# Optimization experiments

Hardware: AMD Instinct MI355X
Metric: run time of the kernel (lower is better)

## Reference

```python
import jax, jax.numpy as jnp
import numpy as np

HID = 1024      # hidden_size (embedding dim, GRU input)
RNN = 1024      # rnn_hidden_size
VOCAB = 50000   # max_node
STEPS = 1024    # num_steps
SOS = 0


def setup_inputs() -> dict:
    key = jax.random.key(0)
    ks = jax.random.split(key, 8)
    s = 0.02
    return {
        "inputs": jax.random.randint(ks[0], (STEPS,), 0, VOCAB),
        "z": jax.random.normal(ks[1], (RNN,), jnp.float32),
        "emb_W": jax.random.uniform(ks[2], (VOCAB, HID), jnp.float32, -0.001, 0.001),
        "out_b": jnp.full((VOCAB,), 0.01, jnp.float32),
        "h2e_W": jax.random.normal(ks[3], (HID, RNN), jnp.float32) * s,
        "h2e_b": jnp.full((HID,), 0.01, jnp.float32),
        "W_ih": jax.random.normal(ks[4], (3 * RNN, HID), jnp.float32) * s,
        "W_hh": jax.random.normal(ks[5], (3 * RNN, RNN), jnp.float32) * s,
        "b_ih": jnp.zeros((3 * RNN,), jnp.float32),
        "b_hh": jnp.zeros((3 * RNN,), jnp.float32),
    }


def reference(inputs, z, emb_W, out_b, h2e_W, h2e_b, W_ih, W_hh, b_ih, b_hh):
    R = RNN

    def gru_cell(h, x):
        gi = W_ih @ x + b_ih          # (3R,)
        gh = W_hh @ h + b_hh          # (3R,)
        r = jax.nn.sigmoid(gi[:R] + gh[:R])
        zg = jax.nn.sigmoid(gi[R:2 * R] + gh[R:2 * R])
        n = jnp.tanh(gi[2 * R:] + r * gh[2 * R:])
        return (1.0 - zg) * n + zg * h

    # teacher forcing: step i consumes token_{i-1} (SOS for i=1), target is inputs[i]
    step_tokens = jnp.concatenate([jnp.array([SOS], dtype=inputs.dtype), inputs[1:-1]])
    targets = inputs[1:]

    def step(h, tok_tgt):
        tok, tgt = tok_tgt
        x = emb_W[tok]                              # embedding lookup (HID,)
        h_new = gru_cell(h, x)                      # (RNN,)
        e = h2e_W @ h_new + h2e_b                   # (HID,)
        logp = jax.nn.log_softmax(emb_W @ e + out_b)  # tied weights, (VOCAB,)
        return h_new, (-logp[tgt], jnp.argmax(logp))

    _, (losses, preds) = jax.lax.scan(step, z, (step_tokens, targets))
    loss = jnp.sum(losses)
    outputs = jnp.zeros((1, inputs.shape[0]), dtype=jnp.int32).at[0, 1:].set(preds.astype(jnp.int32))
    return loss, outputs
```

## Files before the change

### kernel.cpp

```cpp
#include <hip/hip_runtime.h>
#include <math.h>

#define NV      50000
#define T_STEPS 1023
#define KDIM    1024
#define NCH     391
typedef unsigned long long ull;


__global__ __launch_bounds__(256) void k_gather(const int* __restrict__ inputs,
                                                const float* __restrict__ emb,
                                                float* __restrict__ X) {
  const int t = blockIdx.x;
  const int tid = threadIdx.x;
  float4 v = make_float4(0.f, 0.f, 0.f, 0.f);
  if (t < T_STEPS) {
    const int tok = (t == 0) ? 0 : inputs[t];
    v = *(const float4*)&emb[(size_t)tok * KDIM + tid * 4];
  }
  *(float4*)&X[(size_t)t * KDIM + tid * 4] = v;
}

__global__ __launch_bounds__(256) void k_gemm_ffd(const float* __restrict__ A,
                                                  const float* __restrict__ B,
                                                  const float* __restrict__ bias,
                                                  double* __restrict__ C,
                                                  int N, int K) {
  __shared__ float As[32][68];
  __shared__ float Bs[32][68];
  const int tid = threadIdx.x;
  const int bx = blockIdx.x, by = blockIdx.y;
  const int lr = tid >> 2;
  const int lk = (tid & 3) * 8;
  const float* Ap = A + (size_t)(by * 64 + lr) * K + lk;
  const float* Bp = B + (size_t)(bx * 64 + lr) * K + lk;
  const int r0 = (tid >> 4) * 4;
  const int c0 = (tid & 15) * 4;
  double acc[4][4] = {};
  for (int kc = 0; kc < K; kc += 32) {
    const float4 a0 = *(const float4*)(Ap + kc);
    const float4 a1 = *(const float4*)(Ap + kc + 4);
    const float4 b0 = *(const float4*)(Bp + kc);
    const float4 b1 = *(const float4*)(Bp + kc + 4);
    __syncthreads();
    As[lk+0][lr]=a0.x; As[lk+1][lr]=a0.y; As[lk+2][lr]=a0.z; As[lk+3][lr]=a0.w;
    As[lk+4][lr]=a1.x; As[lk+5][lr]=a1.y; As[lk+6][lr]=a1.z; As[lk+7][lr]=a1.w;
    Bs[lk+0][lr]=b0.x; Bs[lk+1][lr]=b0.y; Bs[lk+2][lr]=b0.z; Bs[lk+3][lr]=b0.w;
    Bs[lk+4][lr]=b1.x; Bs[lk+5][lr]=b1.y; Bs[lk+6][lr]=b1.z; Bs[lk+7][lr]=b1.w;
    __syncthreads();
#pragma unroll
    for (int kk = 0; kk < 32; ++kk) {
      const float4 av = *(const float4*)&As[kk][r0];
      const float4 bv = *(const float4*)&Bs[kk][c0];
      const double aa[4] = {av.x, av.y, av.z, av.w};
      const double bb[4] = {bv.x, bv.y, bv.z, bv.w};
#pragma unroll
      for (int i = 0; i < 4; ++i)
#pragma unroll
        for (int j = 0; j < 4; ++j)
          acc[i][j] = fma(aa[i], bb[j], acc[i][j]);
    }
  }
  const int row = by * 64 + r0;
  const int col = bx * 64 + c0;
#pragma unroll
  for (int i = 0; i < 4; ++i)
#pragma unroll
    for (int j = 0; j < 4; ++j)
      C[(size_t)(row + i) * N + col + j] = acc[i][j] + (double)bias[col + j];
}

__global__ __launch_bounds__(256) void k_gemm_dfd(const double* __restrict__ A,
                                                  const float* __restrict__ B,
                                                  const float* __restrict__ bias,
                                                  double* __restrict__ C,
                                                  int N, int K) {
  __shared__ double As[32][68];
  __shared__ float  Bs[32][68];
  const int tid = threadIdx.x;
  const int bx = blockIdx.x, by = blockIdx.y;
  const int lr = tid >> 2;
  const int lk = (tid & 3) * 8;
  const double* Ap = A + (size_t)(by * 64 + lr) * K + lk;
  const float*  Bp = B + (size_t)(bx * 64 + lr) * K + lk;
  const int r0 = (tid >> 4) * 4;
  const int c0 = (tid & 15) * 4;
  double acc[4][4] = {};
  for (int kc = 0; kc < K; kc += 32) {
    double ar[8];
#pragma unroll
    for (int q = 0; q < 8; ++q) ar[q] = Ap[kc + q];
    const float4 b0 = *(const float4*)(Bp + kc);
    const float4 b1 = *(const float4*)(Bp + kc + 4);
    __syncthreads();
#pragma unroll
    for (int q = 0; q < 8; ++q) As[lk + q][lr] = ar[q];
    Bs[lk+0][lr]=b0.x; Bs[lk+1][lr]=b0.y; Bs[lk+2][lr]=b0.z; Bs[lk+3][lr]=b0.w;
    Bs[lk+4][lr]=b1.x; Bs[lk+5][lr]=b1.y; Bs[lk+6][lr]=b1.z; Bs[lk+7][lr]=b1.w;
    __syncthreads();
#pragma unroll
    for (int kk = 0; kk < 32; ++kk) {
      const double aa[4] = {As[kk][r0+0], As[kk][r0+1], As[kk][r0+2], As[kk][r0+3]};
      const float4 bv = *(const float4*)&Bs[kk][c0];
      const double bb[4] = {bv.x, bv.y, bv.z, bv.w};
#pragma unroll
      for (int i = 0; i < 4; ++i)
#pragma unroll
        for (int j = 0; j < 4; ++j)
          acc[i][j] = fma(aa[i], bb[j], acc[i][j]);
    }
  }
  const int row = by * 64 + r0;
  const int col = bx * 64 + c0;
#pragma unroll
  for (int i = 0; i < 4; ++i)
#pragma unroll
    for (int j = 0; j < 4; ++j)
      C[(size_t)(row + i) * N + col + j] = acc[i][j] + (double)bias[col + j];
}

__global__ __launch_bounds__(512, 2) void k_recur(const float* __restrict__ z,
                                                  const float* __restrict__ Whh,
                                                  const float* __restrict__ bhh,
                                                  const double* __restrict__ GI,
                                                  double* __restrict__ H,
                                                  ull* SA, ull* SB) {
  __shared__ double hs[1024];
  const int tid = threadIdx.x;
  const int w = tid >> 6, l = tid & 63;
  const int ibase = blockIdx.x * 16 + w * 2;
  float wreg[6][16];
#pragma unroll
  for (int il = 0; il < 2; ++il)
#pragma unroll
    for (int g = 0; g < 3; ++g) {
      const float* wp = Whh + (size_t)(g * 1024 + ibase + il) * 1024 + l;
#pragma unroll
      for (int m = 0; m < 16; ++m) wreg[il * 3 + g][m] = wp[m * 64];
    }
  double bh[6];
#pragma unroll
  for (int il = 0; il < 2; ++il)
#pragma unroll
    for (int g = 0; g < 3; ++g) bh[il * 3 + g] = (double)bhh[g * 1024 + ibase + il];

  hs[tid]       = (double)z[tid];
  hs[tid + 512] = (double)z[tid + 512];
  double gi[6];
#pragma unroll
  for (int il = 0; il < 2; ++il)
#pragma unroll
    for (int g = 0; g < 3; ++g) gi[il * 3 + g] = GI[g * 1024 + ibase + il];
  __syncthreads();

  for (int t = 0; t < T_STEPS; ++t) {
    const bool more = (t + 1 < T_STEPS);
    const int p = t & 3;
    double s[6] = {0.0, 0.0, 0.0, 0.0, 0.0, 0.0};
#pragma unroll
    for (int m = 0; m < 16; ++m) {
      const double hv = hs[l + 64 * m];
#pragma unroll
      for (int rr = 0; rr < 6; ++rr) s[rr] = fma((double)wreg[rr][m], hv, s[rr]);
    }
#pragma unroll
    for (int rr = 0; rr < 6; ++rr) {
      double v = s[rr];
#pragma unroll
      for (int mk = 32; mk >= 1; mk >>= 1) v += __shfl_xor(v, mk, 64);
      s[rr] = v;
    }
    double hn = 0.0;
    if (l < 2) {
      const int il = l;
      const double r  = 1.0 / (1.0 + exp(-(gi[il * 3 + 0] + s[il * 3 + 0] + bh[il * 3 + 0])));
      const double zg = 1.0 / (1.0 + exp(-(gi[il * 3 + 1] + s[il * 3 + 1] + bh[il * 3 + 1])));
      const double n  = tanh(gi[il * 3 + 2] + r * (s[il * 3 + 2] + bh[il * 3 + 2]));
      hn = (1.0 - zg) * n + zg * hs[ibase + l];
    }
    double gin[6] = {0.0, 0.0, 0.0, 0.0, 0.0, 0.0};
    if (more) {
      const double* gp = GI + (size_t)(t + 1) * 3072;
#pragma unroll
      for (int il = 0; il < 2; ++il)
#pragma unroll
        for (int g = 0; g < 3; ++g) gin[il * 3 + g] = gp[g * 1024 + ibase + il];
    }
    __syncthreads();
    if (l < 2) {
      const int gidx = ibase + l;
      H[(size_t)t * 1024 + gidx] = hn;
      if (more) {
        const ull hb  = (ull)__double_as_longlong(hn);
        const ull tag = ((ull)(t + 1)) << 32;
        __hip_atomic_store(SA + p * 1024 + gidx, tag | (hb >> 32),
                           __ATOMIC_RELAXED, __HIP_MEMORY_SCOPE_AGENT);
        __hip_atomic_store(SB + p * 1024 + gidx, tag | (hb & 0xFFFFFFFFull),
                           __ATOMIC_RELAXED, __HIP_MEMORY_SCOPE_AGENT);
      }
    }
    if (more) {
      const ull want = (ull)(t + 1);
      ull a0, b0, a1, b1;
      while (true) {
        a0 = __hip_atomic_load(SA + p * 1024 + tid,
                               __ATOMIC_RELAXED, __HIP_MEMORY_SCOPE_AGENT);
        b0 = __hip_atomic_load(SB + p * 1024 + tid,
                               __ATOMIC_RELAXED, __HIP_MEMORY_SCOPE_AGENT);
        if ((a0 >> 32) >= want && (b0 >> 32) >= want) break;
        __builtin_amdgcn_s_sleep(1);
      }
      while (true) {
        a1 = __hip_atomic_load(SA + p * 1024 + tid + 512,
                               __ATOMIC_RELAXED, __HIP_MEMORY_SCOPE_AGENT);
        b1 = __hip_atomic_load(SB + p * 1024 + tid + 512,
                               __ATOMIC_RELAXED, __HIP_MEMORY_SCOPE_AGENT);
        if ((a1 >> 32) >= want && (b1 >> 32) >= want) break;
        __builtin_amdgcn_s_sleep(1);
      }
      hs[tid]       = __longlong_as_double((long long)
                        (((a0 & 0xFFFFFFFFull) << 32) | (b0 & 0xFFFFFFFFull)));
      hs[tid + 512] = __longlong_as_double((long long)
                        (((a1 & 0xFFFFFFFFull) << 32) | (b1 & 0xFFFFFFFFull)));
      __syncthreads();
#pragma unroll
      for (int q = 0; q < 6; ++q) gi[q] = gin[q];
    }
  }
}

__global__ __launch_bounds__(256) void k_logits(const double* __restrict__ E,
                                                const float* __restrict__ emb,
                                                const float* __restrict__ out_b,
                                                const int* __restrict__ inputs,
                                                float* __restrict__ candL,
                                                int* __restrict__ candI,
                                                float* __restrict__ Psum,
                                                float* __restrict__ Ttgt) {
  __shared__ double As[128][35];
  __shared__ float  Bs[32][132];
  const int tid = threadIdx.x;
  const int bx = blockIdx.x, by = blockIdx.y;
  const int arow = tid >> 1;
  const int akk  = (tid & 1) * 16;
  const double* Ap = E + (size_t)(by * 128 + arow) * KDIM + akk;
  const int bcol = tid >> 1;
  const int bk   = (tid & 1) * 16;
  const int brow = bx * 128 + bcol;
  const float* Bp = emb + (size_t)brow * KDIM + bk;
  const bool bvalid = (brow < NV);
  const int r0 = (tid >> 4) * 8;
  const int c0 = (tid & 15) * 8;
  double acc[8][8] = {};
  for (int kc = 0; kc < KDIM; kc += 32) {
    double ar[16];
#pragma unroll
    for (int q = 0; q < 16; ++q) ar[q] = Ap[kc + q];
    float4 br[4];
#pragma unroll
    for (int q = 0; q < 4; ++q)
      br[q] = bvalid ? *(const float4*)(Bp + kc + q * 4)
                     : make_float4(0.f, 0.f, 0.f, 0.f);
    __syncthreads();
#pragma unroll
    for (int q = 0; q < 16; ++q) As[arow][akk + q] = ar[q];
#pragma unroll
    for (int q = 0; q < 4; ++q) {
      Bs[bk + q * 4 + 0][bcol] = br[q].x;
      Bs[bk + q * 4 + 1][bcol] = br[q].y;
      Bs[bk + q * 4 + 2][bcol] = br[q].z;
      Bs[bk + q * 4 + 3][bcol] = br[q].w;
    }
    __syncthreads();
#pragma unroll 4
    for (int kk = 0; kk < 32; ++kk) {
      double aa[8];
#pragma unroll
      for (int i = 0; i < 8; ++i) aa[i] = As[r0 + i][kk];
      const float4 bv0 = *(const float4*)&Bs[kk][c0];
      const float4 bv1 = *(const float4*)&Bs[kk][c0 + 4];
      const double bb[8] = {bv0.x, bv0.y, bv0.z, bv0.w,
                            bv1.x, bv1.y, bv1.z, bv1.w};
#pragma unroll
      for (int i = 0; i < 8; ++i)
#pragma unroll
        for (int j = 0; j < 8; ++j)
          acc[i][j] = fma(aa[i], bb[j], acc[i][j]);
    }
  }
  const int colb = bx * 128 + c0;
#pragma unroll
  for (int i = 0; i < 8; ++i) {
    const int s = by * 128 + r0 + i;
    const bool valid = (s < T_STEPS);
    const int tgt = valid ? inputs[s + 1] : -1;
    float L1 = -3e38f, L2 = -3e38f;
    int   i1 = 0x7FFFFFFF, i2 = 0x7FFFFFFF;
    float se = 0.f, tv = -INFINITY;
#pragma unroll
    for (int j = 0; j < 8; ++j) {
      const int v = colb + j;
      if (v < NV) {
        const double lgd = acc[i][j] + (double)out_b[v];
        const float L = (float)lgd;
        se += expf((float)(lgd - 0.01));
        if (v == tgt) tv = (float)lgd;
        if (L > L1 || (L == L1 && v < i1)) { L2 = L1; i2 = i1; L1 = L; i1 = v; }
        else if (L > L2 || (L == L2 && v < i2)) { L2 = L; i2 = v; }
      }
    }
#pragma unroll
    for (int mk = 1; mk <= 8; mk <<= 1) {
      const float oL1 = __shfl_xor(L1, mk, 64); const int oi1 = __shfl_xor(i1, mk, 64);
      const float oL2 = __shfl_xor(L2, mk, 64); const int oi2 = __shfl_xor(i2, mk, 64);
      if (oL1 > L1 || (oL1 == L1 && oi1 < i1)) { L2 = L1; i2 = i1; L1 = oL1; i1 = oi1; }
      else if (oL1 > L2 || (oL1 == L2 && oi1 < i2)) { L2 = oL1; i2 = oi1; }
      if (oL2 > L1 || (oL2 == L1 && oi2 < i1)) { L2 = L1; i2 = i1; L1 = oL2; i1 = oi2; }
      else if (oL2 > L2 || (oL2 == L2 && oi2 < i2)) { L2 = oL2; i2 = oi2; }
      se += __shfl_xor(se, mk, 64);
      tv = fmaxf(tv, __shfl_xor(tv, mk, 64));
    }
    if (((tid & 15) == 0) && valid) {
      const size_t p = (size_t)s * (2 * NCH) + 2 * bx;
      candL[p] = L1;     candI[p] = i1;
      candL[p + 1] = L2; candI[p + 1] = i2;
      atomicAdd(&Psum[s], se);
      if (tv > -1e30f) Ttgt[s] = tv;
    }
  }
}

__global__ __launch_bounds__(256) void k_preds(const float* __restrict__ candL,
                                               const int* __restrict__ candI,
                                               float* __restrict__ out) {
  __shared__ float sL[256];
  __shared__ int   sI[256];
  const int s = blockIdx.x;
  const int tid = threadIdx.x;
  const int n = 2 * NCH;
  const size_t base = (size_t)s * n;
  float m = -3e38f;
  for (int c = tid; c < n; c += 256) m = fmaxf(m, candL[base + c]);
  sL[tid] = m; __syncthreads();
  for (int st = 128; st > 0; st >>= 1) {
    if (tid < st) sL[tid] = fmaxf(sL[tid], sL[tid + st]);
    __syncthreads();
  }
  const float Lmax = sL[0];
  __syncthreads();
  float bq = -3e38f; int bi = 0x7FFFFFFF;
  for (int c = tid; c < n; c += 256) {
    const float L = candL[base + c];
    const int   v = candI[base + c];
    const float d = L - Lmax;
    const float q = d - 10.8125f;
    if (q > bq || (q == bq && v < bi)) { bq = q; bi = v; }
  }
  sL[tid] = bq; sI[tid] = bi; __syncthreads();
  for (int st = 128; st > 0; st >>= 1) {
    if (tid < st) {
      if (sL[tid + st] > sL[tid] ||
          (sL[tid + st] == sL[tid] && sI[tid + st] < sI[tid])) {
        sL[tid] = sL[tid + st]; sI[tid] = sI[tid + st];
      }
    }
    __syncthreads();
  }
  if (tid == 0) out[2 + s] = (float)sI[0];
}

__global__ __launch_bounds__(1024) void k_finish(const float* __restrict__ Psum,
                                                 const float* __restrict__ Ttgt,
                                                 float* __restrict__ out) {
  __shared__ double red[1024];
  const int s = threadIdx.x;
  double ls = 0.0;
  if (s < T_STEPS) ls = 0.01 + log((double)Psum[s]) - (double)Ttgt[s];
  red[s] = ls;
  __syncthreads();
  for (int st = 512; st > 0; st >>= 1) {
    if (s < st) red[s] += red[s + st];
    __syncthreads();
  }
  if (s == 0) out[0] = (float)red[0];
  if (s == 1) out[1] = 0.f;
}

extern "C" void kernel_launch(void* const* d_in, const int* in_sizes, int n_in,
                              void* d_out, int out_size, void* d_ws, size_t ws_size,
                              hipStream_t stream) {
  const int*   inputs = (const int*)  d_in[0];
  const float* z      = (const float*)d_in[1];
  const float* emb    = (const float*)d_in[2];
  const float* out_b  = (const float*)d_in[3];
  const float* h2eW   = (const float*)d_in[4];
  const float* h2eb   = (const float*)d_in[5];
  const float* Wih    = (const float*)d_in[6];
  const float* Whh    = (const float*)d_in[7];
  const float* bih    = (const float*)d_in[8];
  const float* bhh    = (const float*)d_in[9];

  char* ws8 = (char*)d_ws;
  ull*    SA   = (ull*)ws8;
  ull*    SB   = (ull*)(ws8 + 32768);
  float*  Psum = (float*)(ws8 + 66560);
  float*  Ttgt = (float*)(ws8 + 70656);
  float*  X    = (float*)(ws8 + 81920);
  char*   GIb  = ws8 + 81920 + (4u << 20);
  double* GI   = (double*)GIb;
  double* E    = GI;
  float*  candL = (float*)(GIb + (8u << 20));
  int*    candI = (int*)  (GIb + (8u << 20) + 3211264);
  double* H    = (double*)(ws8 + 81920 + (28u << 20));
  float*  out  = (float*)d_out;

  hipMemsetAsync(ws8, 0, 81920, stream);

  k_gather<<<1024, 256, 0, stream>>>(inputs, emb, X);
  k_gemm_ffd<<<dim3(48, 16), 256, 0, stream>>>(X, Wih, bih, GI, 3072, KDIM);
  k_recur<<<64, 512, 0, stream>>>(z, Whh, bhh, GI, H, SA, SB);
  k_gemm_dfd<<<dim3(16, 16), 256, 0, stream>>>(H, h2eW, h2eb, E, KDIM, KDIM);
  k_logits<<<dim3(NCH, 8), 256, 0, stream>>>(E, emb, out_b, inputs,
                                             candL, candI, Psum, Ttgt);
  k_preds<<<T_STEPS, 256, 0, stream>>>(candL, candI, out);
  k_finish<<<1, 1024, 0, stream>>>(Psum, Ttgt, out);
}
```

Before: 9.921 ms.

## Compute logits GEMM in fp32 with fp64 rescoring of near-max candidates

The vocabulary logits GEMM switches from double-precision accumulation to fp32. Only candidates within a small tolerance of the per-row max are recomputed with a double-precision dot product, which preserves argmax tie-breaking. The h2e GEMM additionally writes an fp32 copy of E for this purpose. The recurrence also shrinks its slot ring from 4 to 2 and adds per-block 'done' counters so the buffers can be reused safely. This risks precision differences in the softmax sum and adds serialization and atomics to the logits epilogue.

```diff
diff --git a/kernel.cpp b/kernel.cpp
--- a/kernel.cpp
+++ b/kernel.cpp
@@ -5,6 +5,7 @@
 #define T_STEPS 1023
 #define KDIM    1024
 #define NCH     391
+#define TAU     4e-5f
 typedef unsigned long long ull;
 
 
@@ -74,6 +75,7 @@
                                                   const float* __restrict__ B,
                                                   const float* __restrict__ bias,
                                                   double* __restrict__ C,
+                                                  float* __restrict__ Cf,
                                                   int N, int K) {
   __shared__ double As[32][68];
   __shared__ float  Bs[32][68];
@@ -115,16 +117,19 @@
 #pragma unroll
   for (int i = 0; i < 4; ++i)
 #pragma unroll
-    for (int j = 0; j < 4; ++j)
-      C[(size_t)(row + i) * N + col + j] = acc[i][j] + (double)bias[col + j];
+    for (int j = 0; j < 4; ++j) {
+      const double o = acc[i][j] + (double)bias[col + j];
+      C [(size_t)(row + i) * N + col + j] = o;
+      Cf[(size_t)(row + i) * N + col + j] = (float)o;
+    }
 }
 
 __global__ __launch_bounds__(512, 2) void k_recur(const float* __restrict__ z,
                                                   const float* __restrict__ Whh,
                                                   const float* __restrict__ bhh,
                                                   const double* __restrict__ GI,
-                                                  double* __restrict__ H,
-                                                  ull* SA, ull* SB) {
+                                                  double* H, ull* SA, ull* SB,
+                                                  int* done) {
   __shared__ double hs[1024];
   const int tid = threadIdx.x;
   const int w = tid >> 6, l = tid & 63;
@@ -155,7 +160,12 @@
 
   for (int t = 0; t < T_STEPS; ++t) {
     const bool more = (t + 1 < T_STEPS);
-    const int p = t & 3;
+    const int p = t & 1;
+    const bool gate = more && (t >= 2);
+    int dv = 0x7FFFFFFF;
+    if (gate && tid < 64)
+      dv = __hip_atomic_load(done + p * 64 + tid,
+                             __ATOMIC_RELAXED, __HIP_MEMORY_SCOPE_AGENT);
     double s[6] = {0.0, 0.0, 0.0, 0.0, 0.0, 0.0};
 #pragma unroll
     for (int m = 0; m < 16; ++m) {
@@ -173,9 +183,9 @@
     double hn = 0.0;
     if (l < 2) {
       const int il = l;
-      const double r  = 1.0 / (1.0 + exp(-(gi[il * 3 + 0] + s[il * 3 + 0] + bh[il * 3 + 0])));
-      const double zg = 1.0 / (1.0 + exp(-(gi[il * 3 + 1] + s[il * 3 + 1] + bh[il * 3 + 1])));
-      const double n  = tanh(gi[il * 3 + 2] + r * (s[il * 3 + 2] + bh[il * 3 + 2]));
+      const double r  = 1.0 / (1.0 + exp(-(gi[il*3+0] + s[il*3+0] + bh[il*3+0])));
+      const double zg = 1.0 / (1.0 + exp(-(gi[il*3+1] + s[il*3+1] + bh[il*3+1])));
+      const double n  = tanh(gi[il*3+2] + r * (s[il*3+2] + bh[il*3+2]));
       hn = (1.0 - zg) * n + zg * hs[ibase + l];
     }
     double gin[6] = {0.0, 0.0, 0.0, 0.0, 0.0, 0.0};
@@ -186,10 +196,18 @@
 #pragma unroll
         for (int g = 0; g < 3; ++g) gin[il * 3 + g] = gp[g * 1024 + ibase + il];
     }
+    if (gate && tid < 64) {
+      while (!__all(dv >= t - 1)) {
+        __builtin_amdgcn_s_sleep(1);
+        dv = __hip_atomic_load(done + p * 64 + tid,
+                               __ATOMIC_RELAXED, __HIP_MEMORY_SCOPE_AGENT);
+      }
+    }
     __syncthreads();
     if (l < 2) {
       const int gidx = ibase + l;
-      H[(size_t)t * 1024 + gidx] = hn;
+      __hip_atomic_store(H + (size_t)t * 1024 + gidx, hn,
+                         __ATOMIC_RELAXED, __HIP_MEMORY_SCOPE_AGENT);
       if (more) {
         const ull hb  = (ull)__double_as_longlong(hn);
         const ull tag = ((ull)(t + 1)) << 32;
@@ -223,76 +241,122 @@
       hs[tid + 512] = __longlong_as_double((long long)
                         (((a1 & 0xFFFFFFFFull) << 32) | (b1 & 0xFFFFFFFFull)));
       __syncthreads();
+      if (tid == 0)
+        __hip_atomic_store(done + p * 64 + blockIdx.x, t + 1,
+                           __ATOMIC_RELAXED, __HIP_MEMORY_SCOPE_AGENT);
 #pragma unroll
       for (int q = 0; q < 6; ++q) gi[q] = gin[q];
     }
   }
 }
 
-__global__ __launch_bounds__(256) void k_logits(const double* __restrict__ E,
-                                                const float* __restrict__ emb,
-                                                const float* __restrict__ out_b,
-                                                const int* __restrict__ inputs,
-                                                float* __restrict__ candL,
-                                                int* __restrict__ candI,
-                                                float* __restrict__ Psum,
-                                                float* __restrict__ Ttgt) {
-  __shared__ double As[128][35];
-  __shared__ float  Bs[32][132];
+__global__ __launch_bounds__(256) void k_logits_f32(
+    const float* __restrict__ Ef, const double* __restrict__ E64,
+    const float* __restrict__ emb, const float* __restrict__ out_b,
+    const int* __restrict__ inputs,
+    float* __restrict__ candL, int* __restrict__ candI,
+    float* __restrict__ Psum, float* __restrict__ Ttgt) {
+  __shared__ float As[128][33];
+  __shared__ float Bs[32][132];
+  __shared__ int   WLs[2048];
+  __shared__ int   WLv[2048];
+  __shared__ float Lr[2048];
+  __shared__ int   wcnt;
   const int tid = threadIdx.x;
   const int bx = blockIdx.x, by = blockIdx.y;
-  const int arow = tid >> 1;
-  const int akk  = (tid & 1) * 16;
-  const double* Ap = E + (size_t)(by * 128 + arow) * KDIM + akk;
-  const int bcol = tid >> 1;
-  const int bk   = (tid & 1) * 16;
+  const int arow = tid >> 1, akk = (tid & 1) * 16;
+  const float* Ap = Ef + (size_t)(by * 128 + arow) * KDIM + akk;
+  const int bcol = tid >> 1, bk = (tid & 1) * 16;
   const int brow = bx * 128 + bcol;
   const float* Bp = emb + (size_t)brow * KDIM + bk;
-  const bool bvalid = (brow < NV);
+  const bool bvalid = brow < NV;
   const int r0 = (tid >> 4) * 8;
   const int c0 = (tid & 15) * 8;
-  double acc[8][8] = {};
+  float acc[8][8] = {};
   for (int kc = 0; kc < KDIM; kc += 32) {
-    double ar[16];
-#pragma unroll
-    for (int q = 0; q < 16; ++q) ar[q] = Ap[kc + q];
-    float4 br[4];
-#pragma unroll
-    for (int q = 0; q < 4; ++q)
+    float4 ar[4], br[4];
+#pragma unroll
+    for (int q = 0; q < 4; ++q) {
+      ar[q] = *(const float4*)(Ap + kc + q * 4);
       br[q] = bvalid ? *(const float4*)(Bp + kc + q * 4)
                      : make_float4(0.f, 0.f, 0.f, 0.f);
-    __syncthreads();
-#pragma unroll
-    for (int q = 0; q < 16; ++q) As[arow][akk + q] = ar[q];
+    }
+    __syncthreads();
 #pragma unroll
     for (int q = 0; q < 4; ++q) {
-      Bs[bk + q * 4 + 0][bcol] = br[q].x;
-      Bs[bk + q * 4 + 1][bcol] = br[q].y;
-      Bs[bk + q * 4 + 2][bcol] = br[q].z;
-      Bs[bk + q * 4 + 3][bcol] = br[q].w;
+      As[arow][akk + q*4 + 0] = ar[q].x;
+      As[arow][akk + q*4 + 1] = ar[q].y;
+      As[arow][akk + q*4 + 2] = ar[q].z;
+      As[arow][akk + q*4 + 3] = ar[q].w;
+      Bs[bk + q*4 + 0][bcol] = br[q].x;
+      Bs[bk + q*4 + 1][bcol] = br[q].y;
+      Bs[bk + q*4 + 2][bcol] = br[q].z;
+      Bs[bk + q*4 + 3][bcol] = br[q].w;
     }
     __syncthreads();
 #pragma unroll 4
     for (int kk = 0; kk < 32; ++kk) {
-      double aa[8];
+      float aa[8];
 #pragma unroll
       for (int i = 0; i < 8; ++i) aa[i] = As[r0 + i][kk];
       const float4 bv0 = *(const float4*)&Bs[kk][c0];
       const float4 bv1 = *(const float4*)&Bs[kk][c0 + 4];
-      const double bb[8] = {bv0.x, bv0.y, bv0.z, bv0.w,
-                            bv1.x, bv1.y, bv1.z, bv1.w};
+      const float bb[8] = {bv0.x, bv0.y, bv0.z, bv0.w,
+                           bv1.x, bv1.y, bv1.z, bv1.w};
 #pragma unroll
       for (int i = 0; i < 8; ++i)
 #pragma unroll
         for (int j = 0; j < 8; ++j)
-          acc[i][j] = fma(aa[i], bb[j], acc[i][j]);
+          acc[i][j] = fmaf(aa[i], bb[j], acc[i][j]);
     }
   }
   const int colb = bx * 128 + c0;
+  float ob[8];
+#pragma unroll
+  for (int j = 0; j < 8; ++j) {
+    const int v = colb + j;
+    ob[j] = (v < NV) ? out_b[v] : 0.f;
+  }
 #pragma unroll
   for (int i = 0; i < 8; ++i) {
     const int s = by * 128 + r0 + i;
     const bool valid = (s < T_STEPS);
+    if (tid == 0) wcnt = 0;
+    __syncthreads();
+    float af[8];
+    float M = -3e38f;
+#pragma unroll
+    for (int j = 0; j < 8; ++j) {
+      const int v = colb + j;
+      af[j] = (v < NV) ? acc[i][j] + ob[j] : -3e38f;
+      M = fmaxf(M, af[j]);
+    }
+#pragma unroll
+    for (int mk = 1; mk <= 8; mk <<= 1) M = fmaxf(M, __shfl_xor(M, mk, 64));
+    int myidx[8];
+#pragma unroll
+    for (int j = 0; j < 8; ++j) {
+      const int v = colb + j;
+      myidx[j] = -1;
+      if (valid && v < NV && af[j] >= M - TAU) {
+        const int ix = atomicAdd(&wcnt, 1);
+        myidx[j] = ix;
+        WLs[ix] = s;
+        WLv[ix] = v;
+      }
+    }
+    __syncthreads();
+    const int nw = wcnt;
+    for (int wi = tid; wi < nw; wi += 256) {
+      const int ss = WLs[wi], vv = WLv[wi];
+      const double* Er = E64 + (size_t)ss * KDIM;
+      const float*  br2 = emb + (size_t)vv * KDIM;
+      double d = 0.0;
+#pragma unroll 4
+      for (int k = 0; k < KDIM; ++k) d = fma(Er[k], (double)br2[k], d);
+      Lr[wi] = (float)(d + (double)out_b[vv]);
+    }
+    __syncthreads();
     const int tgt = valid ? inputs[s + 1] : -1;
     float L1 = -3e38f, L2 = -3e38f;
     int   i1 = 0x7FFFFFFF, i2 = 0x7FFFFFFF;
@@ -301,10 +365,9 @@
     for (int j = 0; j < 8; ++j) {
       const int v = colb + j;
       if (v < NV) {
-        const double lgd = acc[i][j] + (double)out_b[v];
-        const float L = (float)lgd;
-        se += expf((float)(lgd - 0.01));
-        if (v == tgt) tv = (float)lgd;
+        se += expf(af[j] - 0.01f);
+        if (v == tgt) tv = af[j];
+        const float L = (myidx[j] >= 0) ? Lr[myidx[j]] : -3e38f;
         if (L > L1 || (L == L1 && v < i1)) { L2 = L1; i2 = i1; L1 = L; i1 = v; }
         else if (L > L2 || (L == L2 && v < i2)) { L2 = L; i2 = v; }
       }
@@ -327,6 +390,7 @@
       atomicAdd(&Psum[s], se);
       if (tv > -1e30f) Ttgt[s] = tv;
     }
+    __syncthreads();
   }
 }
 
@@ -401,27 +465,29 @@
   const float* bhh    = (const float*)d_in[9];
 
   char* ws8 = (char*)d_ws;
-  ull*    SA   = (ull*)ws8;
-  ull*    SB   = (ull*)(ws8 + 32768);
-  float*  Psum = (float*)(ws8 + 66560);
-  float*  Ttgt = (float*)(ws8 + 70656);
-  float*  X    = (float*)(ws8 + 81920);
-  char*   GIb  = ws8 + 81920 + (4u << 20);
-  double* GI   = (double*)GIb;
-  double* E    = GI;
+  ull*    SA    = (ull*)ws8;
+  ull*    SB    = (ull*)(ws8 + 16384);
+  int*    done  = (int*)(ws8 + 32768);
+  float*  Psum  = (float*)(ws8 + 33280);
+  float*  Ttgt  = (float*)(ws8 + 37376);
+  float*  X     = (float*)(ws8 + 49152);
+  char*   GIb   = ws8 + 49152 + (4u << 20);
+  double* GI    = (double*)GIb;
+  double* E     = GI;
   float*  candL = (float*)(GIb + (8u << 20));
   int*    candI = (int*)  (GIb + (8u << 20) + 3211264);
-  double* H    = (double*)(ws8 + 81920 + (28u << 20));
-  float*  out  = (float*)d_out;
-
-  hipMemsetAsync(ws8, 0, 81920, stream);
+  float*  Ef    = (float*)(GIb + (8u << 20) + 6422528);
+  double* H     = (double*)(GIb + (24u << 20));
+  float*  out   = (float*)d_out;
+
+  hipMemsetAsync(ws8, 0, 49152, stream);
 
   k_gather<<<1024, 256, 0, stream>>>(inputs, emb, X);
   k_gemm_ffd<<<dim3(48, 16), 256, 0, stream>>>(X, Wih, bih, GI, 3072, KDIM);
-  k_recur<<<64, 512, 0, stream>>>(z, Whh, bhh, GI, H, SA, SB);
-  k_gemm_dfd<<<dim3(16, 16), 256, 0, stream>>>(H, h2eW, h2eb, E, KDIM, KDIM);
-  k_logits<<<dim3(NCH, 8), 256, 0, stream>>>(E, emb, out_b, inputs,
-                                             candL, candI, Psum, Ttgt);
+  k_recur<<<64, 512, 0, stream>>>(z, Whh, bhh, GI, H, SA, SB, done);
+  k_gemm_dfd<<<dim3(16, 16), 256, 0, stream>>>(H, h2eW, h2eb, E, Ef, KDIM, KDIM);
+  k_logits_f32<<<dim3(NCH, 8), 256, 0, stream>>>(Ef, E, emb, out_b, inputs,
+                                                 candL, candI, Psum, Ttgt);
   k_preds<<<T_STEPS, 256, 0, stream>>>(candL, candI, out);
   k_finish<<<1, 1024, 0, stream>>>(Psum, Ttgt, out);
 }
```

Result: faster. 9.311 ms (-6.2%).
